# Optimization experiments

Hardware: AMD Instinct MI355X
Metric: run time of the kernel (lower is better)

## Reference

```python
import math
import jax, jax.numpy as jnp
import numpy as np
from jax import lax

jax.config.update("jax_enable_x64", True)

DECOMP_LEVEL = 5
# Daubechies-5 (db5) decomposition low-pass filter (pywt convention)
_DB5_LO = np.array([0.003335725285001549, -0.012580751999015526, -0.006241490213011705,
                    0.07757149384006515, -0.03224486958502952, -0.24229488706619015,
                    0.13842814590110342, 0.7243085284385744, 0.6038292697974729,
                    0.160102397974125], dtype=np.float64)
_L = _DB5_LO.size
_DB5_HI = _DB5_LO[::-1].copy() * ((-1.0) ** np.arange(_L))  # QMF high-pass
LO = jnp.asarray(_DB5_LO, jnp.float32)
HI = jnp.asarray(_DB5_HI, jnp.float32)
LOR = jnp.asarray(_DB5_LO[::-1].copy(), jnp.float32)
HIR = jnp.asarray(_DB5_HI[::-1].copy(), jnp.float32)


def _an_last(x):
    # orthonormal periodized analysis along last axis: (..., n) -> (..., n/2) x2
    n = x.shape[-1]
    lead = x.shape[:-1]
    xp = jnp.concatenate([x, x[..., : _L - 2]], axis=-1).reshape(-1, 1, n + _L - 2)
    k = jnp.stack([LO, HI])[:, None, :]  # (2,1,L)
    y = lax.conv_general_dilated(xp, k, (2,), "VALID")  # (B,2,n/2)
    y = y.reshape(lead + (2, n // 2))
    return y[..., 0, :], y[..., 1, :]


def _syn_last(a, d):
    # exact transpose/inverse of _an_last (orthonormal -> W^T = W^-1)
    n2 = a.shape[-1]
    n = 2 * n2
    lead = a.shape[:-1]
    B = int(np.prod(lead)) if lead else 1
    u = jnp.zeros((B, 2, n), a.dtype)
    u = u.at[:, 0, ::2].set(a.reshape(B, n2))
    u = u.at[:, 1, ::2].set(d.reshape(B, n2))
    up = jnp.concatenate([u[..., -(_L - 1):], u], axis=-1)  # circular left pad
    k = jnp.stack([LOR, HIR])[None, :, :]  # (1,2,L)
    y = lax.conv_general_dilated(up, k, (1,), "VALID")  # (B,1,n)
    return y.reshape(lead + (n,))


def _dwt2(x):  # x: (C,h,w) -> ll, lh, hl, hh each (C,h/2,w/2)
    a_h, d_h = _an_last(x.swapaxes(-1, -2))
    a_h = a_h.swapaxes(-1, -2)
    d_h = d_h.swapaxes(-1, -2)
    ll, lh = _an_last(a_h)
    hl, hh = _an_last(d_h)
    return ll, lh, hl, hh


def _idwt2(ll, lh, hl, hh):
    a_h = _syn_last(ll, lh)
    d_h = _syn_last(hl, hh)
    return _syn_last(a_h.swapaxes(-1, -2), d_h.swapaxes(-1, -2)).swapaxes(-1, -2)


def _estimate_noise(data):
    p = data.shape[0]
    rr = data @ data.T
    rri = jnp.linalg.inv(rr + 1e-6 * jnp.eye(p, dtype=data.dtype))
    def per_band(i):
        xx = rri - jnp.outer(rri[:, i], rri[i, :]) / rri[i, i]
        beta = xx @ rr[:, i]
        return beta.at[i].set(0.0)
    betas = jax.vmap(per_band)(jnp.arange(p))  # (p,p)
    return data - betas @ data


def hyres_forward(x):
    H, W, K = x.shape
    N = H * W
    data = x.reshape(N, K).T.astype(jnp.float64)
    w = _estimate_noise(data)
    omega1 = (jnp.sqrt(jnp.var(w, axis=1, ddof=1)) + 1e-30) ** 2  # (K,) f64
    y_w = x * omega1 ** -0.5  # whitened, f64
    u, s, v_pca = jnp.linalg.svd(y_w.reshape(N, K), full_matrices=False)
    pc = (u * s).reshape(W, H, K).astype(jnp.float32).transpose(2, 0, 1)  # (K,H,W)
    # multi-level 2D DWT per channel
    ll = pc
    highs = []
    for _ in range(DECOMP_LEVEL):
        ll, lh, hl, hh = _dwt2(ll)
        highs.append((lh, hl, hh))
    # overwrite-style full coefficient image [[LL,LH],[HL,HH]] recursively
    full = ll
    for lh, hl, hh in reversed(highs):
        top = jnp.concatenate([full, lh], axis=-1)
        bot = jnp.concatenate([hl, hh], axis=-1)
        full = jnp.concatenate([top, bot], axis=-2)
    V = full.transpose(1, 2, 0).reshape(N, K)
    V2 = V * V
    norm_v = jnp.sum(V2)
    n_xyz = jnp.asarray(V.size, jnp.float32)
    col_norm = jnp.sum(V2, axis=0)  # (K,)
    # SURE of soft-threshold over a 15-point grid in [0, sqrt(log N)]
    ts = np.linspace(0.0, math.sqrt(math.log(N)), 15).astype(np.float32)
    sure_cols = []
    for t in ts:
        t2 = float(t * t)
        s_t = (jnp.sum(jnp.minimum(V2, t2), axis=0)
               + 2.0 * jnp.sum((V2 > t2).astype(jnp.float32), axis=0)
               - col_norm)
        sure_cols.append(s_t)
    sure_all = jnp.stack(sure_cols, axis=1)  # (K,15)
    c_const = norm_v - n_xyz
    # replicate the in-place cumulative update: S_r = sum_{j<r} S_j + sure_r + C
    def step(acc, sure_r):
        s_r = acc + sure_r + c_const
        return acc + s_r, jnp.min(s_r)
    _, min_sure = lax.scan(step, jnp.zeros((15,), jnp.float32), sure_all)
    # early-exit: first rank>1 where min_sure increases; else loop ends at K-1
    cond = min_sure[2:] > min_sure[1:-1]
    rank = jnp.where(jnp.any(cond), 2 + jnp.argmax(cond), K - 1)
    mask = (jnp.arange(K) < rank).astype(jnp.float32)[:, None, None]
    # truncation-to-rank == zeroing channels >= rank (inverse DWT is linear)
    y = ll * mask
    for lh, hl, hh in reversed(highs):
        y = _idwt2(y, lh * mask, hl * mask, hh * mask)
    y_est = y.transpose(1, 2, 0).reshape(N, K)  # zero cols beyond rank
    out = (omega1.astype(jnp.float32) ** 0.5) * (y_est @ v_pca.astype(jnp.float32)).reshape(H, W, K)
    return out


def setup_inputs() -> dict:
    key = jax.random.key(0)
    k1, k2, k3 = jax.random.split(key, 3)
    H = W = 384
    K = 191
    R = 8  # low-rank spectral structure + noise, as HyRes assumes
    a = jax.random.normal(k1, (H * W, R), jnp.float32)
    b = jax.random.normal(k2, (R, K), jnp.float32)
    x = (a @ b) / np.sqrt(R) + 0.1 * jax.random.normal(k3, (H * W, K), jnp.float32)
    return {"x": x.reshape(H, W, K)}


def reference(x):
    return hyres_forward(x)
```

## Files before the change

kernel.cpp:

```cpp
#include <hip/hip_runtime.h>
#include <math.h>

#define K_     191
#define LD     192
#define N_     147456
#define MSUB   16
#define NT     15
#define TRI_N  18336
#define SMEM_CHOL  ((TRI_N + 1056) * 8)
#define SMEM_SOLVE ((TRI_N + 192 + 192 + 192) * 8)
#define SMEM2_SZ (6880 * 8 + 32 * 4 + TRI_N * 4)

#define NPAIR  6
#define NSPLIT 128
#define CHUNK  (N_ / NSPLIT)
#define RSTEP  32

__constant__ float c_lo[10] = {
  0.003335725285001549f, -0.012580751999015526f, -0.006241490213011705f,
  0.07757149384006515f,  -0.03224486958502952f, -0.24229488706619015f,
  0.13842814590110342f,   0.7243085284385744f,   0.6038292697974729f,
  0.160102397974125f };
__constant__ float c_hi[10] = {
  0.160102397974125f,    -0.6038292697974729f,   0.7243085284385744f,
 -0.13842814590110342f,  -0.24229488706619015f,  0.03224486958502952f,
  0.07757149384006515f,   0.006241490213011705f,-0.012580751999015526f,
 -0.003335725285001549f };

__global__ __launch_bounds__(256) void k_colsum(const float* __restrict__ x,
                                                double* __restrict__ m)
{
  int t = threadIdx.x;
  long base = (long)blockIdx.x * 512;
  if (t < K_) {
    double s = 0.0;
    const float* p = x + base * K_ + t;
    for (int r = 0; r < 512; ++r) s += (double)p[(long)r * K_];
    atomicAdd(&m[t], s);
  }
}

__global__ __launch_bounds__(256, 3) void k_rr(const float* __restrict__ x,
                                               double* __restrict__ rrg)
{
  __shared__ double Asd[RSTEP][64];
  __shared__ double Bsd[RSTEP][64];

  const int bid   = blockIdx.x;
  const int split = bid & (NSPLIT - 1);
  const int pair  = bid >> 7;
  const int BI[6] = {0, 0, 0, 1, 1, 2};
  const int BJ[6] = {0, 1, 2, 1, 2, 2};
  const int bi = BI[pair], bj = BJ[pair];
  const int ca = bi * 64, cb = bj * 64;

  const int t  = threadIdx.x;
  const int tx = t & 15, ty = t >> 4;
  const long n0 = (long)split * CHUNK;

  double acc[4][4];
  #pragma unroll
  for (int v = 0; v < 4; ++v)
    #pragma unroll
    for (int u = 0; u < 4; ++u) acc[v][u] = 0.0;

  for (int r0 = 0; r0 < CHUNK; r0 += RSTEP) {
    for (int s = t; s < RSTEP * 16; s += 256) {
      int row = s >> 4, g = s & 15;
      long gr = (n0 + r0 + row) * (long)K_;
      int c4a = ca + g * 4, c4b = cb + g * 4;
      #pragma unroll
      for (int e = 0; e < 4; ++e) {
        Asd[row][g * 4 + e] = (c4a + e < K_) ? (double)x[gr + c4a + e] : 0.0;
        Bsd[row][g * 4 + e] = (c4b + e < K_) ? (double)x[gr + c4b + e] : 0.0;
      }
    }
    __syncthreads();
    #pragma unroll 4
    for (int k = 0; k < RSTEP; ++k) {
      double a0 = Asd[k][ty],      a1 = Asd[k][ty + 16];
      double a2 = Asd[k][ty + 32], a3 = Asd[k][ty + 48];
      double b0 = Bsd[k][tx],      b1 = Bsd[k][tx + 16];
      double b2 = Bsd[k][tx + 32], b3 = Bsd[k][tx + 48];
      acc[0][0] += a0 * b0; acc[0][1] += a0 * b1; acc[0][2] += a0 * b2; acc[0][3] += a0 * b3;
      acc[1][0] += a1 * b0; acc[1][1] += a1 * b1; acc[1][2] += a1 * b2; acc[1][3] += a1 * b3;
      acc[2][0] += a2 * b0; acc[2][1] += a2 * b1; acc[2][2] += a2 * b2; acc[2][3] += a2 * b3;
      acc[3][0] += a3 * b0; acc[3][1] += a3 * b1; acc[3][2] += a3 * b2; acc[3][3] += a3 * b3;
    }
    __syncthreads();
  }

  #pragma unroll
  for (int v = 0; v < 4; ++v) {
    int mrow = ca + ty + 16 * v;
    #pragma unroll
    for (int u = 0; u < 4; ++u) {
      int ncol = cb + tx + 16 * u;
      if (mrow < K_ && ncol < K_)
        atomicAdd(&rrg[(size_t)mrow * K_ + ncol], acc[v][u]);
    }
  }
}

__global__ __launch_bounds__(256) void k_reduce(const double* __restrict__ rrg,
                                                double* __restrict__ rr)
{
  int idx = blockIdx.x * 256 + threadIdx.x;
  if (idx >= TRI_N) return;
  int i = (int)((sqrtf(8.f * (float)idx + 1.f) - 1.f) * 0.5f);
  while ((i + 1) * (i + 2) / 2 <= idx) ++i;
  while (i * (i + 1) / 2 > idx) --i;
  int j = idx - (i * (i + 1)) / 2;
  double s = rrg[(size_t)j * K_ + i];
  rr[i * LD + j] = s;
  rr[j * LD + i] = s;
}

__global__ __launch_bounds__(512) void k_chol(
    const double* __restrict__ rr, double* __restrict__ Lg,
    double* __restrict__ rdg)
{
  extern __shared__ double smem[];
  double* tri = smem;
  double* tmp = smem + TRI_N;
  const int t = threadIdx.x;

  for (int i = t >> 5; i < K_; i += 16) {
    int base = (i * (i + 1)) / 2;
    for (int j = t & 31; j <= i; j += 32) {
      double v = rr[i * LD + j];
      tri[base + j] = (i == j) ? v + 1e-6 : v;
    }
  }
  __syncthreads();

  for (int J = 0; J < 6; ++J) {
    const int j0 = J * 32;
    const int nb = (K_ - j0 < 32) ? (K_ - j0) : 32;

    if (t < 64) {
      const int rl = t & 31;
      double a[32];
      #pragma unroll
      for (int c = 0; c < 32; ++c) {
        int i = j0 + rl;
        a[c] = (c <= rl && rl < nb) ? tri[(i * (i + 1)) / 2 + j0 + c] : 0.0;
      }
      #pragma unroll
      for (int k = 0; k < 32; ++k) {
        double akk = __shfl(a[k], k);
        double piv = sqrt(akk);
        double inv = 1.0 / piv;
        if (t == k) {
          tmp[k] = inv;
          if (j0 + k < K_) rdg[j0 + k] = inv;
        }
        a[k] = (rl == k) ? piv : a[k] * inv;
        #pragma unroll
        for (int c = k + 1; c < 32; ++c) {
          double lck = __shfl(a[k], c);
          if (c <= rl) a[c] -= a[k] * lck;
        }
      }
      if (t < 32 && rl < nb) {
        int i = j0 + rl;
        int rb = (i * (i + 1)) / 2 + j0;
        #pragma unroll
        for (int c = 0; c < 32; ++c)
          if (c <= rl) tri[rb + c] = a[c];
      }
    }
    __syncthreads();

    {
      int p = j0 + 32 + t;
      if (nb == 32 && p < K_) {
        int pb = (p * (p + 1)) / 2 + j0;
        double v[32];
        #pragma unroll
        for (int c = 0; c < 32; ++c) v[c] = tri[pb + c];
        #pragma unroll
        for (int c = 0; c < 32; ++c) {
          double s = v[c];
          #pragma unroll
          for (int q = 0; q < c; ++q) {
            int cc = j0 + c;
            s -= v[q] * tri[(cc * (cc + 1)) / 2 + j0 + q];
          }
          v[c] = s * tmp[c];
        }
        #pragma unroll
        for (int c = 0; c < 32; ++c) tri[pb + c] = v[c];
      }
    }
    __syncthreads();

    {
      int s0 = j0 + 32;
      int n = K_ - s0;
      if (n > 0) {
        int R4 = (n + 3) >> 2;
        int T4 = R4 * (R4 + 1) / 2;
        for (int tile = t; tile < T4; tile += 512) {
          int ti = (int)((sqrtf(8.f * (float)tile + 1.f) - 1.f) * 0.5f);
          while ((ti + 1) * (ti + 2) / 2 <= tile) ++ti;
          while (ti * (ti + 1) / 2 > tile) --ti;
          int tj = tile - ti * (ti + 1) / 2;
          int r0 = s0 + ti * 4, c0 = s0 + tj * 4;
          int rb[4], cb[4];
          #pragma unroll
          for (int u = 0; u < 4; ++u) {
            int r = (r0 + u < K_) ? r0 + u : K_ - 1;
            rb[u] = (r * (r + 1)) / 2;
            int c = (c0 + u < K_) ? c0 + u : K_ - 1;
            cb[u] = (c * (c + 1)) / 2;
          }
          double acc[4][4];
          #pragma unroll
          for (int u = 0; u < 4; ++u)
            #pragma unroll
            for (int v2 = 0; v2 < 4; ++v2) acc[u][v2] = 0.0;
          #pragma unroll 4
          for (int p = 0; p < 32; ++p) {
            double lr[4], lc[4];
            #pragma unroll
            for (int u = 0; u < 4; ++u) {
              lr[u] = tri[rb[u] + j0 + p];
              lc[u] = tri[cb[u] + j0 + p];
            }
            #pragma unroll
            for (int u = 0; u < 4; ++u)
              #pragma unroll
              for (int v2 = 0; v2 < 4; ++v2) acc[u][v2] += lr[u] * lc[v2];
          }
          #pragma unroll
          for (int u = 0; u < 4; ++u) {
            int r = r0 + u;
            if (r < K_) {
              #pragma unroll
              for (int v2 = 0; v2 < 4; ++v2) {
                int c = c0 + v2;
                if (c <= r) tri[rb[u] + c] -= acc[u][v2];
              }
            }
          }
        }
      }
    }
    __syncthreads();
  }

  for (int idx = t; idx < TRI_N; idx += 512) Lg[idx] = tri[idx];
}

__global__ __launch_bounds__(256) void k_csolve(
    const double* __restrict__ Lg, const double* __restrict__ rdg,
    const double* __restrict__ mg, double* __restrict__ s2g,
    double* __restrict__ zg)
{
  extern __shared__ double ssm[];
  double* Ls   = ssm;
  double* rd_s = Ls + TRI_N;
  double* m_sh = rd_s + 192;
  double* ys   = m_sh + 192;
  const int t = threadIdx.x;
  const int bid = blockIdx.x;

  const int start = (bid < K_) ? (bid * (bid + 1)) / 2 : 0;
  for (int idx = start + t; idx < TRI_N; idx += 256) Ls[idx] = Lg[idx];
  if (t < K_) { rd_s[t] = rdg[t]; m_sh[t] = mg[t]; }
  __syncthreads();

  if (t >= 64) return;
  const int l = t;

  if (bid < K_) {
    const int i = bid;
    double x0 = 0.0, x1 = 0.0, x2 = 0.0;
    {
      double rdi = rd_s[i];
      if ((i & 63) == l) {
        int sl = i >> 6;
        if (sl == 0) x0 = rdi; else if (sl == 1) x1 = rdi; else x2 = rdi;
      }
    }
    for (int r = i + 1; r < K_; ++r) {
      int rb = (r * (r + 1)) >> 1;
      double partial = 0.0;
      { int k = l;       if (k < r) partial += Ls[rb + k] * x0; }
      { int k = l + 64;  if (k < r) partial += Ls[rb + k] * x1; }
      { int k = l + 128; if (k < r) partial += Ls[rb + k] * x2; }
      #pragma unroll
      for (int mm = 32; mm > 0; mm >>= 1) partial += __shfl_xor(partial, mm);
      double val = -partial * rd_s[r];
      if ((r & 63) == l) {
        int sl = r >> 6;
        if (sl == 0) x0 = val; else if (sl == 1) x1 = val; else x2 = val;
      }
    }
    double s2p = x0 * x0 + x1 * x1 + x2 * x2;
    #pragma unroll
    for (int mm = 32; mm > 0; mm >>= 1) s2p += __shfl_xor(s2p, mm);
    if (l == 0) s2g[i] = s2p;
  } else {
    double y0 = 0.0, y1 = 0.0, y2 = 0.0;
    for (int r = 0; r < K_; ++r) {
      int rb = (r * (r + 1)) >> 1;
      double partial = 0.0;
      { int k = l;       if (k < r) partial += Ls[rb + k] * y0; }
      { int k = l + 64;  if (k < r) partial += Ls[rb + k] * y1; }
      { int k = l + 128; if (k < r) partial += Ls[rb + k] * y2; }
      #pragma unroll
      for (int mm = 32; mm > 0; mm >>= 1) partial += __shfl_xor(partial, mm);
      double val = (m_sh[r] - partial) * rd_s[r];
      if ((r & 63) == l) {
        int sl = r >> 6;
        if (sl == 0) y0 = val; else if (sl == 1) y1 = val; else y2 = val;
      }
      if (l == 0) ys[r] = val;
    }
    double z0 = 0.0, z1 = 0.0, z2 = 0.0;
    for (int r = K_ - 1; r >= 0; --r) {
      double partial = 0.0;
      { int k = l;       if (k > r && k < K_) partial += Ls[((k * (k + 1)) >> 1) + r] * z0; }
      { int k = l + 64;  if (k > r && k < K_) partial += Ls[((k * (k + 1)) >> 1) + r] * z1; }
      { int k = l + 128; if (k > r && k < K_) partial += Ls[((k * (k + 1)) >> 1) + r] * z2; }
      #pragma unroll
      for (int mm = 32; mm > 0; mm >>= 1) partial += __shfl_xor(partial, mm);
      double val = (ys[r] - partial) * rd_s[r];
      if ((r & 63) == l) {
        int sl = r >> 6;
        if (sl == 0) z0 = val; else if (sl == 1) z1 = val; else z2 = val;
      }
      if (l == 0) zg[r] = val;
    }
  }
}

__global__ __launch_bounds__(256) void k_finals(
    const double* __restrict__ rr, const double* __restrict__ s2g,
    const double* __restrict__ zg, double* __restrict__ invsq,
    float* __restrict__ normv)
{
  __shared__ double tmps[K_];
  const int t = threadIdx.x;
  if (t < K_) {
    double dii = s2g[t];
    double q = 1.0 / dii;
    double sm_ = zg[t] / dii;
    double var = (q - sm_ * sm_ / (double)N_) / (double)(N_ - 1);
    double t1 = sqrt(var) + 1e-30;
    double om = t1 * t1;
    invsq[t] = 1.0 / sqrt(om);
    tmps[t] = rr[t * LD + t] / om;
  }
  __syncthreads();
  if (t < 64) {
    double s = 0.0;
    for (int i = t; i < K_; i += 64) s += tmps[i];
    #pragma unroll
    for (int off = 32; off > 0; off >>= 1) s += __shfl_down(s, off);
    if (t == 0) *normv = (float)s;
  }
}

__device__ __forceinline__ void cholqr(double* shQ, double* shS, int t)
{
  if (t < MSUB * MSUB) {
    int a = t & (MSUB - 1), b = t >> 4;
    double s = 0.0;
    for (int r = 0; r < K_; ++r) s += shQ[r * MSUB + a] * shQ[r * MSUB + b];
    shS[b * 17 + a] = s;
  }
  __syncthreads();
  for (int k = 0; k < MSUB; ++k) {
    if (t == 0) shS[k * 17 + k] = sqrt(shS[k * 17 + k]);
    __syncthreads();
    if (t > k && t < MSUB) shS[t * 17 + k] /= shS[k * 17 + k];
    __syncthreads();
    if (t < MSUB * MSUB) {
      int r = t & (MSUB - 1), c = t >> 4;
      if (c > k && r >= c) shS[r * 17 + c] -= shS[r * 17 + k] * shS[c * 17 + k];
    }
    __syncthreads();
  }
  if (t < K_) {
    double q[MSUB];
    #pragma unroll
    for (int c = 0; c < MSUB; ++c) {
      double v = shQ[t * MSUB + c];
      for (int p = 0; p < c; ++p) v -= q[p] * shS[c * 17 + p];
      q[c] = v / shS[c * 17 + c];
    }
    #pragma unroll
    for (int c = 0; c < MSUB; ++c) shQ[t * MSUB + c] = q[c];
  }
  __syncthreads();
}

__global__ __launch_bounds__(512) void k_sub(
    const double* __restrict__ rr, const double* __restrict__ invsq,
    float* __restrict__ W1, float* __restrict__ W2)
{
  extern __shared__ double dsm[];
  double* shQ  = dsm;
  double* shZ  = shQ + 3056;
  double* shS  = shZ + 3056;
  double* Ws   = shS + 272;
  double* inv_s= Ws + 272;
  double* ev   = inv_s + 192;
  double* cs_  = ev + 16;
  double* sn_  = cs_ + 8;
  int* ipp  = (int*)(sn_ + 8);
  int* iqq  = ipp + 8;
  int* perm = iqq + 8;
  float* tri = (float*)(perm + 16);
  const int t = threadIdx.x;

  if (t < K_) inv_s[t] = invsq[t];
  __syncthreads();
  for (int i = t >> 4; i < K_; i += 32) {
    int base = (i * (i + 1)) / 2;
    double di = inv_s[i];
    for (int j = t & 15; j <= i; j += 16)
      tri[base + j] = (float)(rr[i * LD + j] * di * inv_s[j]);
  }
  __syncthreads();

  for (int idx = t; idx < K_ * MSUB; idx += 512) {
    int i = idx >> 4, c = idx & 15;
    float g = (i >= c) ? tri[(i * (i + 1)) / 2 + c] : tri[(c * (c + 1)) / 2 + i];
    shQ[idx] = (double)g;
  }
  __syncthreads();

  cholqr(shQ, shS, t);
  for (int it = 0; it < 4; ++it) {
    for (int idx = t; idx < K_ * MSUB; idx += 512) shZ[idx] = shQ[idx];
    __syncthreads();
    if (t < 96 * 4) {
      int i2 = t >> 2, c4 = t & 3;
      int r0 = 2 * i2, r1 = r0 + 1;
      int has1 = (r1 < K_);
      int rb0 = (r0 * (r0 + 1)) >> 1;
      int rb1 = has1 ? ((r1 * (r1 + 1)) >> 1) : rb0;
      int cb0 = c4 * 4;
      double s0a = 0.0, s0b = 0.0, s0c = 0.0, s0d = 0.0;
      double s1a = 0.0, s1b = 0.0, s1c = 0.0, s1d = 0.0;
      #pragma unroll 2
      for (int k = 0; k <= r0; ++k) {
        double g0 = (double)tri[rb0 + k];
        double g1 = (double)tri[rb1 + k];
        double za = shZ[k * MSUB + cb0],     zb = shZ[k * MSUB + cb0 + 1];
        double zc = shZ[k * MSUB + cb0 + 2], zd = shZ[k * MSUB + cb0 + 3];
        s0a += g0 * za; s0b += g0 * zb; s0c += g0 * zc; s0d += g0 * zd;
        s1a += g1 * za; s1b += g1 * zb; s1c += g1 * zc; s1d += g1 * zd;
      }
      if (has1) {
        double g0 = (double)tri[rb1 + r0];
        double g1 = (double)tri[rb1 + r1];
        double za = shZ[r1 * MSUB + cb0],     zb = shZ[r1 * MSUB + cb0 + 1];
        double zc = shZ[r1 * MSUB + cb0 + 2], zd = shZ[r1 * MSUB + cb0 + 3];
        s0a += g0 * za; s0b += g0 * zb; s0c += g0 * zc; s0d += g0 * zd;
        s1a += g1 * za; s1b += g1 * zb; s1c += g1 * zc; s1d += g1 * zd;
      }
      int kk = ((r1 + 1) * (r1 + 2)) >> 1;
      #pragma unroll 2
      for (int k = r1 + 1; k < K_; ++k) {
        double g0 = (double)tri[kk + r0];
        double g1 = (double)tri[kk + r1];
        double za = shZ[k * MSUB + cb0],     zb = shZ[k * MSUB + cb0 + 1];
        double zc = shZ[k * MSUB + cb0 + 2], zd = shZ[k * MSUB + cb0 + 3];
        s0a += g0 * za; s0b += g0 * zb; s0c += g0 * zc; s0d += g0 * zd;
        s1a += g1 * za; s1b += g1 * zb; s1c += g1 * zc; s1d += g1 * zd;
        kk += k + 1;
      }
      shQ[r0 * MSUB + cb0]     = s0a;
      shQ[r0 * MSUB + cb0 + 1] = s0b;
      shQ[r0 * MSUB + cb0 + 2] = s0c;
      shQ[r0 * MSUB + cb0 + 3] = s0d;
      if (has1) {
        shQ[r1 * MSUB + cb0]     = s1a;
        shQ[r1 * MSUB + cb0 + 1] = s1b;
        shQ[r1 * MSUB + cb0 + 2] = s1c;
        shQ[r1 * MSUB + cb0 + 3] = s1d;
      }
    }
    __syncthreads();
    if (it < 3) cholqr(shQ, shS, t);
  }
  if (t < MSUB * MSUB) {
    int a = t & 15, b = t >> 4;
    double s = 0.0;
    for (int r = 0; r < K_; ++r) s += shZ[r * MSUB + b] * shQ[r * MSUB + a];
    shS[b * 17 + a] = s;
  }
  if (t < MSUB * 17) Ws[t] = 0.0;
  __syncthreads();
  if (t < MSUB) Ws[t * 17 + t] = 1.0;
  __syncthreads();
  for (int sweep = 0; sweep < 6; ++sweep) {
    for (int round = 0; round < 15; ++round) {
      if (t < 8) {
        int ia = (t == 0) ? 0 : (1 + ((t - 1 + round) % 15));
        int ib = 1 + ((14 - t + round) % 15);
        int p = ia < ib ? ia : ib;
        int q = ia < ib ? ib : ia;
        double app = shS[p * 17 + p], aqq = shS[q * 17 + q], apq = shS[p * 17 + q];
        double c = 1.0, s = 0.0;
        if (fabs(apq) > 1e-30 * (fabs(app) + fabs(aqq)) && apq != 0.0) {
          double tau = (aqq - app) / (2.0 * apq);
          double tt = (tau >= 0.0 ? 1.0 : -1.0) / (fabs(tau) + sqrt(1.0 + tau * tau));
          c = 1.0 / sqrt(1.0 + tt * tt); s = tt * c;
        }
        cs_[t] = c; sn_[t] = s; ipp[t] = p; iqq[t] = q;
      }
      __syncthreads();
      if (t < 128) {
        int i = t & 15, mI = t >> 4;
        int p = ipp[mI], q = iqq[mI];
        double c = cs_[mI], s = sn_[mI];
        double u = shS[i * 17 + p], v = shS[i * 17 + q];
        shS[i * 17 + p] = c * u - s * v; shS[i * 17 + q] = s * u + c * v;
        double wu = Ws[i * 17 + p], wv = Ws[i * 17 + q];
        Ws[i * 17 + p] = c * wu - s * wv; Ws[i * 17 + q] = s * wu + c * wv;
      }
      __syncthreads();
      if (t < 128) {
        int j = t & 15, mI = t >> 4;
        int p = ipp[mI], q = iqq[mI];
        double c = cs_[mI], s = sn_[mI];
        double u = shS[p * 17 + j], v = shS[q * 17 + j];
        shS[p * 17 + j] = c * u - s * v; shS[q * 17 + j] = s * u + c * v;
      }
      __syncthreads();
    }
  }
  if (t == 0) {
    for (int i = 0; i < MSUB; ++i) { ev[i] = shS[i * 17 + i]; perm[i] = i; }
    for (int i = 0; i < MSUB; ++i) {
      int best = i;
      for (int j = i + 1; j < MSUB; ++j)
        if (ev[perm[j]] > ev[perm[best]]) best = j;
      int tp = perm[i]; perm[i] = perm[best]; perm[best] = tp;
    }
  }
  __syncthreads();
  for (int idx = t; idx < K_ * MSUB; idx += 512) {
    int i = idx >> 4, c = idx & 15;
    int pc_ = perm[c];
    double e = 0.0;
    #pragma unroll
    for (int p = 0; p < MSUB; ++p) e += shZ[i * MSUB + p] * Ws[p * 17 + pc_];
    W1[i * MSUB + c] = (float)(inv_s[i] * e);
    W2[c * K_ + i]   = (float)(e / inv_s[i]);
  }
}

__global__ __launch_bounds__(256) void k_pc(const float* __restrict__ x,
                                            const float* __restrict__ W1,
                                            float* __restrict__ pc)
{
  __shared__ float xs[32][192];
  __shared__ float w1s[K_ * MSUB];
  int t = threadIdx.x;
  long n0 = (long)blockIdx.x * 32;
  for (int idx = t; idx < K_ * MSUB; idx += 256) w1s[idx] = W1[idx];
  for (int idx = t; idx < 32 * K_; idx += 256) {
    int row = idx / K_, col = idx - row * K_;
    xs[row][col] = x[(n0 + row) * K_ + col];
  }
  __syncthreads();
  int c = t & 15, nl = t >> 4;
  float a0 = 0.f, a1 = 0.f;
  for (int k = 0; k < K_; ++k) {
    float w = w1s[k * MSUB + c];
    a0 += xs[nl][k] * w;
    a1 += xs[nl + 16][k] * w;
  }
  __syncthreads();
  float* ts = &xs[0][0];
  ts[c * 33 + nl]      = a0;
  ts[c * 33 + nl + 16] = a1;
  __syncthreads();
  for (int idx = t; idx < MSUB * 32; idx += 256) {
    int cc = idx >> 5, nn = idx & 31;
    pc[(size_t)cc * N_ + n0 + nn] = ts[cc * 33 + nn];
  }
}

__global__ __launch_bounds__(256) void k_dwtv(const float* __restrict__ in,
                                              float* __restrict__ outv, int s)
{
  long gid = (long)blockIdx.x * 256 + threadIdx.x;
  int h = s >> 1;
  long per = (long)h * s;
  if (gid >= MSUB * per) return;
  int ch = (int)(gid / per);
  long rem = gid - (long)ch * per;
  int r = (int)(rem / s);
  int col = (int)(rem - (long)r * s);
  const float* cin = in + (long)ch * s * s;
  float la = 0.f, ld_ = 0.f;
  int base = 2 * r;
  #pragma unroll
  for (int l = 0; l < 10; ++l) {
    int rr_ = base + l; if (rr_ >= s) rr_ -= s;
    float v = cin[(long)rr_ * s + col];
    la += c_lo[l] * v; ld_ += c_hi[l] * v;
  }
  float* cout = outv + (long)ch * s * s;
  cout[(long)r * s + col] = la;
  cout[(long)(h + r) * s + col] = ld_;
}

__global__ __launch_bounds__(256) void k_dwth(const float* __restrict__ inv,
                                              float* __restrict__ llout,
                                              float* __restrict__ coef,
                                              int s, long offL, int last)
{
  long gid = (long)blockIdx.x * 256 + threadIdx.x;
  int h = s >> 1;
  long per = (long)s * h;
  if (gid >= MSUB * per) return;
  int ch = (int)(gid / per);
  long rem = gid - (long)ch * per;
  int r = (int)(rem / h);
  int mcol = (int)(rem - (long)r * h);
  const float* row = inv + (long)ch * s * s + (long)r * s;
  float lo = 0.f, hi = 0.f;
  int base = 2 * mcol;
  #pragma unroll
  for (int l = 0; l < 10; ++l) {
    int cc = base + l; if (cc >= s) cc -= s;
    float v = row[cc];
    lo += c_lo[l] * v; hi += c_hi[l] * v;
  }
  float* cslab = coef + (size_t)ch * N_ + offL;
  if (r < h) {
    llout[(size_t)ch * h * h + (long)r * h + mcol] = lo;
    if (last) coef[(size_t)ch * N_ + 147312 + (long)r * h + mcol] = lo;
    cslab[(long)r * h + mcol] = hi;
  } else {
    int rd = r - h;
    cslab[(long)h * h + (long)rd * h + mcol] = lo;
    cslab[(long)2 * h * h + (long)rd * h + mcol] = hi;
  }
}

__global__ __launch_bounds__(256) void k_stats(const float* __restrict__ coef,
                                               float* __restrict__ stats)
{
  int ch = blockIdx.x;
  int t = threadIdx.x;
  float T2[NT];
  {
    double stop = sqrt(log(147456.0));
    double step = stop / 14.0;
    for (int i = 0; i < NT; ++i) {
      double td = (i == 14) ? stop : (double)i * step;
      float tf = (float)td;
      T2[i] = tf * tf;
    }
  }
  float cn = 0.f, sm[NT], ct[NT];
  #pragma unroll
  for (int i = 0; i < NT; ++i) { sm[i] = 0.f; ct[i] = 0.f; }
  const float* base = coef + (size_t)ch * N_;
  for (int idx = t; idx < N_; idx += 256) {
    float v = base[idx];
    float v2 = v * v;
    cn += v2;
    #pragma unroll
    for (int i = 0; i < NT; ++i) {
      sm[i] += fminf(v2, T2[i]);
      ct[i] += (v2 > T2[i]) ? 1.0f : 0.0f;
    }
  }
  __shared__ float red2[4][32];
  int lane = t & 63, wv = t >> 6;
  for (int a = 0; a < 31; ++a) {
    float val = (a == 0) ? cn : ((a < 16) ? sm[a - 1] : ct[a - 16]);
    #pragma unroll
    for (int off = 32; off > 0; off >>= 1) val += __shfl_down(val, off);
    if (lane == 0) red2[wv][a] = val;
  }
  __syncthreads();
  if (t < 31)
    stats[ch * 31 + t] = red2[0][t] + red2[1][t] + red2[2][t] + red2[3][t];
}

__global__ void k_rank(const float* __restrict__ stats,
                       const float* __restrict__ normv, int* __restrict__ rankp)
{
  if (threadIdx.x != 0 || blockIdx.x != 0) return;
  float c_const = *normv - 28164096.0f;
  float acc[NT];
  for (int i = 0; i < NT; ++i) acc[i] = 0.f;
  float minsure[MSUB];
  for (int r = 0; r < MSUB; ++r) {
    float cn = stats[r * 31 + 0];
    float mn = 3.4e38f;
    for (int i = 0; i < NT; ++i) {
      float sure = stats[r * 31 + 1 + i] + 2.0f * stats[r * 31 + 16 + i] - cn;
      float s_r = acc[i] + sure + c_const;
      acc[i] = acc[i] + s_r;
      if (s_r < mn) mn = s_r;
    }
    minsure[r] = mn;
  }
  int rank = -1;
  for (int r = 2; r < MSUB; ++r) {
    if (minsure[r] > minsure[r - 1]) { rank = r; break; }
  }
  if (rank < 0) rank = MSUB - 1;
  *rankp = rank;
}

__global__ __launch_bounds__(256) void k_out(const float* __restrict__ pc,
                                             const float* __restrict__ W2,
                                             const int* __restrict__ rankp,
                                             float* __restrict__ out)
{
  long gid = (long)blockIdx.x * 256 + threadIdx.x;
  int n = (int)(gid / K_);
  int j = (int)(gid - (long)n * K_);
  int rank = *rankp;
  float acc = 0.f;
  for (int c = 0; c < rank; ++c)
    acc += pc[(size_t)c * N_ + n] * W2[c * K_ + j];
  out[gid] = acc;
}

extern "C" void kernel_launch(void* const* d_in, const int* in_sizes, int n_in,
                              void* d_out, int out_size, void* d_ws, size_t ws_size,
                              hipStream_t stream)
{
  if (n_in < 1 || in_sizes[0] != N_ * K_) return;
  const float* x = (const float*)d_in[0];
  float* out = (float*)d_out;
  (void)out_size;

  char* w = (char*)d_ws;
  size_t off = 0;
  auto alloc = [&](size_t bytes) -> char* {
    char* p = w + off;
    off = (off + bytes + 255) & ~(size_t)255;
    return p;
  };
  double* m_    = (double*)alloc(K_ * 8);
  double* rrp   = (double*)alloc((size_t)K_ * K_ * 8);
  double* rr    = (double*)alloc((size_t)K_ * LD * 8);
  double* Lg    = (double*)alloc((size_t)TRI_N * 8);
  double* rdg   = (double*)alloc(192 * 8);
  double* s2g   = (double*)alloc(192 * 8);
  double* zg    = (double*)alloc(192 * 8);
  double* invsq = (double*)alloc(K_ * 8);
  float*  normv = (float*)alloc(256);
  float*  W1    = (float*)alloc((size_t)K_ * MSUB * 4);
  float*  W2    = (float*)alloc((size_t)MSUB * K_ * 4);
  float*  pc    = (float*)alloc((size_t)MSUB * N_ * 4);
  float*  tmpv  = (float*)alloc((size_t)MSUB * N_ * 4);
  float*  coef  = (float*)alloc((size_t)MSUB * N_ * 4);
  float*  curA  = (float*)alloc((size_t)MSUB * 192 * 192 * 4);
  float*  curB  = (float*)alloc((size_t)MSUB * 96 * 96 * 4);
  float*  stats = (float*)alloc((size_t)MSUB * 31 * 4);
  int*    rankp = (int*)alloc(256);
  if (off > ws_size) return;

  hipMemsetAsync(m_, 0, K_ * sizeof(double), stream);
  hipMemsetAsync(rrp, 0, (size_t)K_ * K_ * sizeof(double), stream);

  hipFuncSetAttribute(reinterpret_cast<const void*>(k_chol),
                      hipFuncAttributeMaxDynamicSharedMemorySize, SMEM_CHOL);
  hipFuncSetAttribute(reinterpret_cast<const void*>(k_csolve),
                      hipFuncAttributeMaxDynamicSharedMemorySize, SMEM_SOLVE);
  hipFuncSetAttribute(reinterpret_cast<const void*>(k_sub),
                      hipFuncAttributeMaxDynamicSharedMemorySize, SMEM2_SZ);

  k_colsum<<<N_ / 512, 256, 0, stream>>>(x, m_);
  k_rr<<<NPAIR * NSPLIT, 256, 0, stream>>>(x, rrp);
  k_reduce<<<(TRI_N + 255) / 256, 256, 0, stream>>>(rrp, rr);
  k_chol<<<1, 512, SMEM_CHOL, stream>>>(rr, Lg, rdg);
  k_csolve<<<K_ + 1, 256, SMEM_SOLVE, stream>>>(Lg, rdg, m_, s2g, zg);
  k_finals<<<1, 256, 0, stream>>>(rr, s2g, zg, invsq, normv);
  k_sub<<<1, 512, SMEM2_SZ, stream>>>(rr, invsq, W1, W2);
  k_pc<<<N_ / 32, 256, 0, stream>>>(x, W1, pc);

  int   sizes[5] = {384, 192, 96, 48, 24};
  long  offs[5]  = {0, 110592, 138240, 145152, 146880};
  float* lls[5]  = {curA, curB, curA, curB, curA};
  const float* curin = pc;
  for (int lev = 0; lev < 5; ++lev) {
    int s = sizes[lev], h = s >> 1;
    long nth = (long)MSUB * h * s;
    k_dwtv<<<(int)((nth + 255) / 256), 256, 0, stream>>>(curin, tmpv, s);
    k_dwth<<<(int)((nth + 255) / 256), 256, 0, stream>>>(tmpv, lls[lev], coef,
                                                         s, offs[lev],
                                                         lev == 4 ? 1 : 0);
    curin = lls[lev];
  }

  k_stats<<<MSUB, 256, 0, stream>>>(coef, stats);
  k_rank<<<1, 64, 0, stream>>>(stats, normv, rankp);
  k_out<<<(N_ * K_) / 256, 256, 0, stream>>>(pc, W2, rankp, out);
}
```

Measured before the change: 1.476 ms.

## Fuse column-sum into Gram kernel, reuse A tile on diagonal blocks, retune split

Removes the separate column-mean kernel and computes the column sums inside the Gram (x^T x) kernel's diagonal-block blocks, so x is not streamed an extra time. Diagonal blocks now load only one tile and use it for both operands, halving their global loads. The loader is reorganised so each thread loads one column of consecutive rows. The split count doubles and the row step halves, with higher occupancy bounds, trading more atomic adds into the Gram buffer for more parallelism and smaller shared-memory tiles.

```diff
diff --git a/kernel.cpp b/kernel.cpp
--- a/kernel.cpp
+++ b/kernel.cpp
@@ -12,9 +12,9 @@
 #define SMEM2_SZ (6880 * 8 + 32 * 4 + TRI_N * 4)
 
 #define NPAIR  6
-#define NSPLIT 128
+#define NSPLIT 256
 #define CHUNK  (N_ / NSPLIT)
-#define RSTEP  32
+#define RSTEP  16
 
 __constant__ float c_lo[10] = {
   0.003335725285001549f, -0.012580751999015526f, -0.006241490213011705f,
@@ -27,35 +27,25 @@
   0.07757149384006515f,   0.006241490213011705f,-0.012580751999015526f,
  -0.003335725285001549f };
 
-__global__ __launch_bounds__(256) void k_colsum(const float* __restrict__ x,
-                                                double* __restrict__ m)
-{
-  int t = threadIdx.x;
-  long base = (long)blockIdx.x * 512;
-  if (t < K_) {
-    double s = 0.0;
-    const float* p = x + base * K_ + t;
-    for (int r = 0; r < 512; ++r) s += (double)p[(long)r * K_];
-    atomicAdd(&m[t], s);
-  }
-}
-
-__global__ __launch_bounds__(256, 3) void k_rr(const float* __restrict__ x,
-                                               double* __restrict__ rrg)
+__global__ __launch_bounds__(256, 6) void k_rr(const float* __restrict__ x,
+                                               double* __restrict__ rrg,
+                                               double* __restrict__ m)
 {
   __shared__ double Asd[RSTEP][64];
   __shared__ double Bsd[RSTEP][64];
 
   const int bid   = blockIdx.x;
   const int split = bid & (NSPLIT - 1);
-  const int pair  = bid >> 7;
+  const int pair  = bid >> 8;
   const int BI[6] = {0, 0, 0, 1, 1, 2};
   const int BJ[6] = {0, 1, 2, 1, 2, 2};
   const int bi = BI[pair], bj = BJ[pair];
+  const int diag = (bi == bj);
   const int ca = bi * 64, cb = bj * 64;
 
   const int t  = threadIdx.x;
   const int tx = t & 15, ty = t >> 4;
+  const int mycol = t & 63, rowgrp = t >> 6;
   const long n0 = (long)split * CHUNK;
 
   double acc[4][4];
@@ -63,25 +53,31 @@
   for (int v = 0; v < 4; ++v)
     #pragma unroll
     for (int u = 0; u < 4; ++u) acc[v][u] = 0.0;
+  double csum = 0.0;
 
   for (int r0 = 0; r0 < CHUNK; r0 += RSTEP) {
-    for (int s = t; s < RSTEP * 16; s += 256) {
-      int row = s >> 4, g = s & 15;
+    #pragma unroll
+    for (int rr_ = 0; rr_ < RSTEP; rr_ += 4) {
+      int row = rr_ + rowgrp;
       long gr = (n0 + r0 + row) * (long)K_;
-      int c4a = ca + g * 4, c4b = cb + g * 4;
-      #pragma unroll
-      for (int e = 0; e < 4; ++e) {
-        Asd[row][g * 4 + e] = (c4a + e < K_) ? (double)x[gr + c4a + e] : 0.0;
-        Bsd[row][g * 4 + e] = (c4b + e < K_) ? (double)x[gr + c4b + e] : 0.0;
-      }
-    }
-    __syncthreads();
+      int c = ca + mycol;
+      double va = (c < K_) ? (double)x[gr + c] : 0.0;
+      Asd[row][mycol] = va;
+      if (diag) {
+        csum += va;
+      } else {
+        int c2 = cb + mycol;
+        Bsd[row][mycol] = (c2 < K_) ? (double)x[gr + c2] : 0.0;
+      }
+    }
+    __syncthreads();
+    const double (*Bs)[64] = diag ? Asd : Bsd;
     #pragma unroll 4
     for (int k = 0; k < RSTEP; ++k) {
       double a0 = Asd[k][ty],      a1 = Asd[k][ty + 16];
       double a2 = Asd[k][ty + 32], a3 = Asd[k][ty + 48];
-      double b0 = Bsd[k][tx],      b1 = Bsd[k][tx + 16];
-      double b2 = Bsd[k][tx + 32], b3 = Bsd[k][tx + 48];
+      double b0 = Bs[k][tx],       b1 = Bs[k][tx + 16];
+      double b2 = Bs[k][tx + 32],  b3 = Bs[k][tx + 48];
       acc[0][0] += a0 * b0; acc[0][1] += a0 * b1; acc[0][2] += a0 * b2; acc[0][3] += a0 * b3;
       acc[1][0] += a1 * b0; acc[1][1] += a1 * b1; acc[1][2] += a1 * b2; acc[1][3] += a1 * b3;
       acc[2][0] += a2 * b0; acc[2][1] += a2 * b1; acc[2][2] += a2 * b2; acc[2][3] += a2 * b3;
@@ -98,6 +94,19 @@
       int ncol = cb + tx + 16 * u;
       if (mrow < K_ && ncol < K_)
         atomicAdd(&rrg[(size_t)mrow * K_ + ncol], acc[v][u]);
+    }
+  }
+
+  if (diag) {
+    ((double*)Bsd)[t] = csum;
+    __syncthreads();
+    if (t < 64) {
+      int c = ca + t;
+      if (c < K_) {
+        double s = ((double*)Bsd)[t] + ((double*)Bsd)[t + 64] +
+                   ((double*)Bsd)[t + 128] + ((double*)Bsd)[t + 192];
+        atomicAdd(&m[c], s);
+      }
     }
   }
 }
@@ -778,8 +787,7 @@
   hipFuncSetAttribute(reinterpret_cast<const void*>(k_sub),
                       hipFuncAttributeMaxDynamicSharedMemorySize, SMEM2_SZ);
 
-  k_colsum<<<N_ / 512, 256, 0, stream>>>(x, m_);
-  k_rr<<<NPAIR * NSPLIT, 256, 0, stream>>>(x, rrp);
+  k_rr<<<NPAIR * NSPLIT, 256, 0, stream>>>(x, rrp, m_);
   k_reduce<<<(TRI_N + 255) / 256, 256, 0, stream>>>(rrp, rr);
   k_chol<<<1, 512, SMEM_CHOL, stream>>>(rr, Lg, rdg);
   k_csolve<<<K_ + 1, 256, SMEM_SOLVE, stream>>>(Lg, rdg, m_, s2g, zg);
```

New measurement: 1.424 ms. 3.5% less time.
